# Kernel optimization log

Measured on AMD Instinct MI355X. Metric: run time of the kernel, lower is better.

Reference implementation:

```python
import jax, jax.numpy as jnp
import numpy as np
from jax import lax

EPS = 1e-6
D_MODEL = 2048
N_HEADS = 32
D_STATE = 64
HEADDIM = D_MODEL // N_HEADS  # 64, d_inner = expand*d_model = 2048
D_CONV = 4
INTER = 5504


def rmsnorm(x, w, eps=EPS):
    v = jnp.mean(jnp.square(x.astype(jnp.float32)), axis=-1, keepdims=True)
    return (x.astype(jnp.float32) * lax.rsqrt(v + eps)).astype(x.dtype) * w


def ssm_scan(x, dt, Bm, Cm):
    # x: (b,l,h,p) unscaled; dt: (b,l,h); Bm,Cm: (b,l,h,n)
    # DiscreteMamba2: h_t = exp(-dt_t) h_{t-1} + x_t (x) B_t ; y_t = h_t . C_t
    # (mamba_chunk_scan is called with x/dt and A=-1, so dt*(x/dt)=x)
    a = jnp.exp(-dt)  # (b,l,h)
    b, l, h, p = x.shape
    n = Bm.shape[-1]

    def step(hst, inp):
        a_t, x_t, B_t, C_t = inp
        hst = a_t[..., None, None] * hst + jnp.einsum('bhp,bhn->bhpn', x_t, B_t)
        y = jnp.einsum('bhpn,bhn->bhp', hst, C_t)
        return hst, y

    h0 = jnp.zeros((b, h, p, n), dtype=x.dtype)
    xs = (jnp.moveaxis(a, 1, 0), jnp.moveaxis(x, 1, 0),
          jnp.moveaxis(Bm, 1, 0), jnp.moveaxis(Cm, 1, 0))
    _, ys = lax.scan(step, h0, xs)
    return jnp.moveaxis(ys, 0, 1)  # (b,l,h,p)


def setup_inputs() -> dict:
    key = jax.random.key(0)
    ks = jax.random.split(key, 8)
    s = 0.02
    d_inner = D_MODEL
    conv_dim = d_inner + 2 * N_HEADS * D_STATE  # 6144
    d_in_proj = 2 * d_inner + 2 * N_HEADS * D_STATE + N_HEADS  # 8224
    return {
        'hidden_states': jax.random.normal(ks[0], (2, 2048, D_MODEL), jnp.float32),
        'attention_mask': jnp.ones((2, 2048), jnp.float32),
        'in_proj_w': jax.random.normal(ks[1], (d_in_proj, D_MODEL), jnp.float32) * s,
        'conv_w': jax.random.normal(ks[2], (conv_dim, 1, D_CONV), jnp.float32) * s,
        'conv_b': jnp.zeros((conv_dim,), jnp.float32),
        'z_bias': jnp.zeros((d_inner,), jnp.float32),
        'D': jnp.ones((N_HEADS,), jnp.float32),
        'out_proj_w': jax.random.normal(ks[3], (D_MODEL, d_inner), jnp.float32) * s,
        'ln1_w': jnp.ones((D_MODEL,), jnp.float32),
        'ln2_w': jnp.ones((D_MODEL,), jnp.float32),
        'gate_w': jax.random.normal(ks[4], (INTER, D_MODEL), jnp.float32) * s,
        'up_w': jax.random.normal(ks[5], (INTER, D_MODEL), jnp.float32) * s,
        'down_w': jax.random.normal(ks[6], (D_MODEL, INTER), jnp.float32) * s,
    }


def reference(hidden_states, attention_mask, in_proj_w, conv_w, conv_b, z_bias,
              D, out_proj_w, ln1_w, ln2_w, gate_w, up_w, down_w):
    b, l, d_model = hidden_states.shape
    d_inner = z_bias.shape[0]
    h_heads = D.shape[0]
    conv_dim = conv_w.shape[0]
    d_state = (conv_dim - d_inner) // (2 * h_heads)
    headdim = d_inner // h_heads

    residual = hidden_states
    h = rmsnorm(hidden_states, ln1_w)
    h = h * attention_mask[..., None]

    # --- DiscreteMamba2 mixer ---
    zxbcdt = jnp.einsum('bld,ed->ble', h, in_proj_w)
    z = zxbcdt[..., :d_inner]
    xBC = zxbcdt[..., d_inner:d_inner + conv_dim]
    A_log = zxbcdt[..., d_inner + conv_dim:]  # (b,l,h)

    # causal depthwise conv (activation = identity)
    xc = jnp.pad(jnp.swapaxes(xBC, 1, 2), ((0, 0), (0, 0), (conv_w.shape[-1] - 1, 0)))
    xBC = lax.conv_general_dilated(xc, conv_w, (1,), 'VALID',
                                   dimension_numbers=('NCH', 'OIH', 'NCH'),
                                   feature_group_count=conv_dim)
    xBC = jnp.swapaxes(xBC + conv_b[None, :, None], 1, 2)  # (b,l,conv_dim)

    x = xBC[..., :d_inner].reshape(b, l, h_heads, headdim)
    Bm = xBC[..., d_inner:d_inner + h_heads * d_state].reshape(b, l, h_heads, d_state)
    Cm = xBC[..., d_inner + h_heads * d_state:].reshape(b, l, h_heads, d_state)

    dt = jax.nn.softplus(A_log)  # (b,l,h)
    y = ssm_scan(x, dt, Bm, Cm)
    y = y + D[None, None, :, None] * x  # D skip uses unscaled x
    y = y.reshape(b, l, d_inner)

    gated = y * jax.nn.silu(z + z_bias)
    mixer_out = jnp.einsum('bld,ed->ble', gated, out_proj_w)

    h = mixer_out + residual
    residual2 = h
    h = rmsnorm(h, ln2_w)
    mlp = jnp.einsum('bli,di->bld',
                     jax.nn.silu(jnp.einsum('bld,id->bli', h, gate_w)) *
                     jnp.einsum('bld,id->bli', h, up_w),
                     down_w)
    return residual2 + mlp
```

## Files before the change

### kernel.cpp

```cpp
#include <hip/hip_runtime.h>
#include <math.h>

typedef __bf16 bf16_t;
typedef __attribute__((ext_vector_type(8))) __bf16 bf16x8;
typedef __attribute__((ext_vector_type(4))) float f32x4;

#define D_MODEL   2048
#define L_SEQ     2048
#define BATCH     2
#define NTOK      4096
#define N_HEADS   32
#define D_STATE   64
#define HEADDIM   64
#define D_INNER   2048
#define CONV_DIM  6144
#define D_IN_PROJ 8224
#define INTER     5504
#define QCHUNK    128
#define KCHUNKS   16

__device__ __forceinline__ void gld_lds16(const void* g, void* l) {
    __builtin_amdgcn_global_load_lds(
        (const __attribute__((address_space(1))) unsigned int*)g,
        (__attribute__((address_space(3))) unsigned int*)l, 16, 0, 0);
}

__global__ __launch_bounds__(256) void cvt_kernel(
    const float* __restrict__ s, bf16_t* __restrict__ d, int n8)
{
    int i = blockIdx.x * 256 + threadIdx.x;
    if (i >= n8) return;
    const float4* s4 = (const float4*)s;
    float4 a = s4[2 * i], b = s4[2 * i + 1];
    bf16x8 r;
    r[0] = (bf16_t)a.x; r[1] = (bf16_t)a.y; r[2] = (bf16_t)a.z; r[3] = (bf16_t)a.w;
    r[4] = (bf16_t)b.x; r[5] = (bf16_t)b.y; r[6] = (bf16_t)b.z; r[7] = (bf16_t)b.w;
    ((bf16x8*)d)[i] = r;
}

__global__ __launch_bounds__(256) void rmsnorm_kernel(
    const float* __restrict__ x, const float* __restrict__ w,
    const float* __restrict__ mask, bf16_t* __restrict__ out)
{
    __shared__ float red[4];
    __shared__ float sinv;
    int row = blockIdx.x;
    const float* xr = x + (size_t)row * D_MODEL;
    float xv[8];
    float ss = 0.f;
#pragma unroll
    for (int i = 0; i < 8; ++i) {
        float v = xr[threadIdx.x + 256 * i];
        xv[i] = v;
        ss += v * v;
    }
    for (int off = 32; off >= 1; off >>= 1) ss += __shfl_down(ss, off, 64);
    int lane = threadIdx.x & 63, wv = threadIdx.x >> 6;
    if (lane == 0) red[wv] = ss;
    __syncthreads();
    if (threadIdx.x == 0) {
        float t = red[0] + red[1] + red[2] + red[3];
        sinv = rsqrtf(t / (float)D_MODEL + 1e-6f);
    }
    __syncthreads();
    float s = sinv;
    float m = mask ? mask[row] : 1.f;
    bf16_t* orow = out + (size_t)row * D_MODEL;
#pragma unroll
    for (int i = 0; i < 8; ++i) {
        int c = threadIdx.x + 256 * i;
        orow[c] = (bf16_t)(xv[i] * s * w[c] * m);
    }
}

template <bool RES, typename OT>
__global__ __launch_bounds__(256) void gemm_bt(
    const bf16_t* __restrict__ X, const bf16_t* __restrict__ W,
    const float* __restrict__ R, OT* __restrict__ O,
    int N, int K)
{
    __shared__ __attribute__((aligned(16))) bf16_t As[128 * 32];
    __shared__ __attribute__((aligned(16))) bf16_t Bs[128 * 32];

    int tid = threadIdx.x;
    int m0 = blockIdx.y * 128;
    int n0 = blockIdx.x * 128;

    f32x4 acc[4][4] = {};

    int lane = tid & 63;
    int wv = tid >> 6;
    int wm = (wv >> 1) * 64, wn = (wv & 1) * 64;
    int lm = lane & 15, lq = lane >> 4;

    int srow = tid >> 2;
    int scol = (tid & 3) * 8;
    const bf16_t* Xp0 = X + (size_t)(m0 + srow) * K + scol;
    const bf16_t* Xp1 = X + (size_t)(m0 + 64 + srow) * K + scol;
    int wr0 = n0 + srow;      if (wr0 > N - 1) wr0 = N - 1;
    int wr1 = n0 + 64 + srow; if (wr1 > N - 1) wr1 = N - 1;
    const bf16_t* Wp0 = W + (size_t)wr0 * K + scol;
    const bf16_t* Wp1 = W + (size_t)wr1 * K + scol;
    bf16_t* lA0 = &As[tid * 8];
    bf16_t* lA1 = &As[2048 + tid * 8];
    bf16_t* lB0 = &Bs[tid * 8];
    bf16_t* lB1 = &Bs[2048 + tid * 8];

    for (int k0 = 0; k0 < K; k0 += 32) {
        __syncthreads();
        gld_lds16(Xp0 + k0, lA0);
        gld_lds16(Xp1 + k0, lA1);
        gld_lds16(Wp0 + k0, lB0);
        gld_lds16(Wp1 + k0, lB1);
        __syncthreads();

        bf16x8 a[4], b[4];
#pragma unroll
        for (int i = 0; i < 4; ++i)
            a[i] = *(const bf16x8*)&As[(wm + i * 16 + lm) * 32 + lq * 8];
#pragma unroll
        for (int i = 0; i < 4; ++i)
            b[i] = *(const bf16x8*)&Bs[(wn + i * 16 + lm) * 32 + lq * 8];
#pragma unroll
        for (int mi = 0; mi < 4; ++mi)
#pragma unroll
            for (int ni = 0; ni < 4; ++ni)
                acc[mi][ni] = __builtin_amdgcn_mfma_f32_16x16x32_bf16(
                    a[mi], b[ni], acc[mi][ni], 0, 0, 0);
    }

#pragma unroll
    for (int mi = 0; mi < 4; ++mi)
#pragma unroll
        for (int ni = 0; ni < 4; ++ni) {
            int n = n0 + wn + ni * 16 + lm;
            if (n >= N) continue;
            int mbase = m0 + wm + mi * 16 + lq * 4;
#pragma unroll
            for (int r = 0; r < 4; ++r) {
                size_t off = (size_t)(mbase + r) * N + n;
                float v = acc[mi][ni][r];
                if (RES) v += R[off];
                O[off] = (OT)v;
            }
        }
}

__global__ __launch_bounds__(256) void conv_kernel(
    const bf16_t* __restrict__ zx, const float* __restrict__ cw,
    const float* __restrict__ cb, bf16_t* __restrict__ out)
{
    int c = blockIdx.x * 256 + threadIdx.x;
    int l0 = blockIdx.y * 128;
    int b = blockIdx.z;
    float w0 = cw[c * 4 + 0], w1 = cw[c * 4 + 1];
    float w2 = cw[c * 4 + 2], w3 = cw[c * 4 + 3];
    float bias = cb[c];
    const bf16_t* src = zx + (size_t)b * L_SEQ * D_IN_PROJ + 2048 + c;
    bf16_t* dst = out + (size_t)b * L_SEQ * CONV_DIM + c;
    float xm3 = (l0 >= 3) ? (float)src[(size_t)(l0 - 3) * D_IN_PROJ] : 0.f;
    float xm2 = (l0 >= 2) ? (float)src[(size_t)(l0 - 2) * D_IN_PROJ] : 0.f;
    float xm1 = (l0 >= 1) ? (float)src[(size_t)(l0 - 1) * D_IN_PROJ] : 0.f;
    for (int l = l0; l < l0 + 128; ++l) {
        float xc = (float)src[(size_t)l * D_IN_PROJ];
        float r = bias + xm3 * w0 + xm2 * w1 + xm1 * w2 + xc * w3;
        dst[(size_t)l * CONV_DIM] = (bf16_t)r;
        xm3 = xm2; xm2 = xm1; xm1 = xc;
    }
}

__global__ __launch_bounds__(256) void scan_state_kernel(
    const bf16_t* __restrict__ conv, const bf16_t* __restrict__ zx,
    float* __restrict__ Schunk, float* __restrict__ Aprod)
{
    const int SS = 32;
    __shared__ __attribute__((aligned(16))) float xs[SS][64];
    __shared__ __attribute__((aligned(16))) float bs[SS][64];
    __shared__ float as_[SS];

    int k = blockIdx.x, h = blockIdx.y, b = blockIdx.z;
    int tid = threadIdx.x, lane = tid & 63, wv = tid >> 6;
    int pt = tid >> 3, nt = tid & 7;
    int p0 = pt * 2, n0 = nt * 8;

    float st0[8] = {0, 0, 0, 0, 0, 0, 0, 0};
    float st1[8] = {0, 0, 0, 0, 0, 0, 0, 0};
    float aprod = 1.f;

    const bf16_t* cbase = conv + (size_t)b * L_SEQ * CONV_DIM + h * 64;
    const bf16_t* abase = zx + (size_t)b * L_SEQ * D_IN_PROJ + 8192 + h;

    int tstart = k * QCHUNK;
    for (int t0 = tstart; t0 < tstart + QCHUNK; t0 += SS) {
        int soff = (wv >> 1) * 16;
        for (int s = 0; s < 16; ++s) {
            size_t row = (size_t)(t0 + soff + s);
            if ((wv & 1) == 0) xs[soff + s][lane] = (float)cbase[row * CONV_DIM + lane];
            else               bs[soff + s][lane] = (float)cbase[row * CONV_DIM + 2048 + lane];
        }
        if (tid < SS) {
            float v = (float)abase[(size_t)(t0 + tid) * D_IN_PROJ];
            as_[tid] = 1.f / (1.f + __expf(v));
        }
        __syncthreads();
        for (int s = 0; s < SS; ++s) {
            float a = as_[s];
            float x0 = xs[s][p0], x1 = xs[s][p0 + 1];
            aprod *= a;
#pragma unroll
            for (int j = 0; j < 8; ++j) {
                float Bv = bs[s][n0 + j];
                st0[j] = a * st0[j] + x0 * Bv;
                st1[j] = a * st1[j] + x1 * Bv;
            }
        }
        __syncthreads();
    }
    size_t base = (((size_t)(b * N_HEADS + h)) * KCHUNKS + k) * 4096;
    float4* d0 = (float4*)&Schunk[base + p0 * 64 + n0];
    d0[0] = make_float4(st0[0], st0[1], st0[2], st0[3]);
    d0[1] = make_float4(st0[4], st0[5], st0[6], st0[7]);
    float4* d1 = (float4*)&Schunk[base + (p0 + 1) * 64 + n0];
    d1[0] = make_float4(st1[0], st1[1], st1[2], st1[3]);
    d1[1] = make_float4(st1[4], st1[5], st1[6], st1[7]);
    if (tid == 0) Aprod[(b * N_HEADS + h) * KCHUNKS + k] = aprod;
}

__global__ __launch_bounds__(256) void scan_combine_kernel(
    const float* __restrict__ Schunk, const float* __restrict__ Aprod,
    float* __restrict__ Sinit)
{
    int bh = blockIdx.x >> 4;
    int e = (blockIdx.x & 15) * 256 + threadIdx.x;
    size_t base = (size_t)bh * KCHUNKS * 4096 + e;
    float S = 0.f;
    for (int k = 0; k < KCHUNKS; ++k) {
        Sinit[base + (size_t)k * 4096] = S;
        float ap = Aprod[bh * KCHUNKS + k];
        S = ap * S + Schunk[base + (size_t)k * 4096];
    }
}

__global__ __launch_bounds__(256) void scan_out_kernel(
    const bf16_t* __restrict__ conv, const bf16_t* __restrict__ zx,
    const float* __restrict__ Sinit, const float* __restrict__ Dp,
    const float* __restrict__ zb, bf16_t* __restrict__ gated)
{
    const int S = 16;
    __shared__ __attribute__((aligned(16))) float xs[S][64];
    __shared__ __attribute__((aligned(16))) float bs[S][64];
    __shared__ __attribute__((aligned(16))) float cs[S][64];
    __shared__ __attribute__((aligned(16))) float zs[S][64];
    __shared__ float as_[S];

    int k = blockIdx.x, h = blockIdx.y, b = blockIdx.z;
    int tid = threadIdx.x;
    int lane = tid & 63, wv = tid >> 6;
    int pt = tid >> 3, nt = tid & 7;
    int p0 = pt * 2, n0 = nt * 8;

    size_t sbase = (((size_t)(b * N_HEADS + h)) * KCHUNKS + k) * 4096;
    float4 v00 = *(const float4*)&Sinit[sbase + p0 * 64 + n0];
    float4 v01 = *(const float4*)&Sinit[sbase + p0 * 64 + n0 + 4];
    float4 v10 = *(const float4*)&Sinit[sbase + (p0 + 1) * 64 + n0];
    float4 v11 = *(const float4*)&Sinit[sbase + (p0 + 1) * 64 + n0 + 4];
    float st0[8] = {v00.x, v00.y, v00.z, v00.w, v01.x, v01.y, v01.z, v01.w};
    float st1[8] = {v10.x, v10.y, v10.z, v10.w, v11.x, v11.y, v11.z, v11.w};

    float Dh  = Dp[h];
    float zb0 = zb[h * 64 + p0];
    float zb1 = zb[h * 64 + p0 + 1];

    const bf16_t* cbase = conv + (size_t)b * L_SEQ * CONV_DIM + h * 64;
    const bf16_t* zbase = zx + (size_t)b * L_SEQ * D_IN_PROJ + h * 64;
    const bf16_t* abase = zx + (size_t)b * L_SEQ * D_IN_PROJ + 8192 + h;
    bf16_t* obase = gated + (size_t)b * L_SEQ * D_INNER + h * 64;

    int tstart = k * QCHUNK;
    for (int t0 = tstart; t0 < tstart + QCHUNK; t0 += S) {
        for (int s = 0; s < S; ++s) {
            size_t row = (size_t)(t0 + s);
            if (wv == 0)      xs[s][lane] = (float)cbase[row * CONV_DIM + lane];
            else if (wv == 1) bs[s][lane] = (float)cbase[row * CONV_DIM + 2048 + lane];
            else if (wv == 2) cs[s][lane] = (float)cbase[row * CONV_DIM + 4096 + lane];
            else              zs[s][lane] = (float)zbase[row * D_IN_PROJ + lane];
        }
        if (tid < S) {
            float v = (float)abase[(size_t)(t0 + tid) * D_IN_PROJ];
            as_[tid] = 1.f / (1.f + __expf(v));
        }
        __syncthreads();

        for (int s = 0; s < S; ++s) {
            float a = as_[s];
            float x0 = xs[s][p0], x1 = xs[s][p0 + 1];
            float part0 = 0.f, part1 = 0.f;
#pragma unroll
            for (int j = 0; j < 8; ++j) {
                float Bv = bs[s][n0 + j];
                float Cv = cs[s][n0 + j];
                st0[j] = a * st0[j] + x0 * Bv;
                st1[j] = a * st1[j] + x1 * Bv;
                part0 += st0[j] * Cv;
                part1 += st1[j] * Cv;
            }
            for (int o = 1; o < 8; o <<= 1) {
                part0 += __shfl_xor(part0, o, 64);
                part1 += __shfl_xor(part1, o, 64);
            }
            if (nt == 0) {
                float y0 = part0 + Dh * x0;
                float y1 = part1 + Dh * x1;
                float z0 = zs[s][p0] + zb0;
                float z1 = zs[s][p0 + 1] + zb1;
                y0 *= z0 / (1.f + __expf(-z0));
                y1 *= z1 / (1.f + __expf(-z1));
                bf16_t* o2 = obase + (size_t)(t0 + s) * D_INNER + p0;
                o2[0] = (bf16_t)y0;
                o2[1] = (bf16_t)y1;
            }
        }
        __syncthreads();
    }
}

__global__ __launch_bounds__(256) void act_kernel(
    const bf16x8* __restrict__ g, const bf16x8* __restrict__ u,
    bf16x8* __restrict__ act, int n8)
{
    int i = blockIdx.x * 256 + threadIdx.x;
    if (i >= n8) return;
    bf16x8 gv = g[i], uv = u[i], r;
#pragma unroll
    for (int j = 0; j < 8; ++j) {
        float x = (float)gv[j];
        r[j] = (bf16_t)((x / (1.f + __expf(-x))) * (float)uv[j]);
    }
    act[i] = r;
}

extern "C" void kernel_launch(void* const* d_in, const int* in_sizes, int n_in,
                              void* d_out, int out_size, void* d_ws, size_t ws_size,
                              hipStream_t stream) {
    const float* hidden     = (const float*)d_in[0];
    const float* mask       = (const float*)d_in[1];
    const float* in_proj_w  = (const float*)d_in[2];
    const float* conv_w     = (const float*)d_in[3];
    const float* conv_b     = (const float*)d_in[4];
    const float* z_bias     = (const float*)d_in[5];
    const float* Dvec       = (const float*)d_in[6];
    const float* out_proj_w = (const float*)d_in[7];
    const float* ln1_w      = (const float*)d_in[8];
    const float* ln2_w      = (const float*)d_in[9];
    const float* gate_w     = (const float*)d_in[10];
    const float* up_w       = (const float*)d_in[11];
    const float* down_w     = (const float*)d_in[12];
    float* out = (float*)d_out;

    char* ws = (char*)d_ws;
    bf16_t* zxb    = (bf16_t*)(ws + 0);
    bf16_t* convo  = (bf16_t*)(ws + 67371008);
    bf16_t* hn     = (bf16_t*)(ws + 117702656);
    bf16_t* gated  = (bf16_t*)(ws + 117702656);
    bf16_t* h2n    = (bf16_t*)(ws + 134479872);
    float*  Schunk = (float*) (ws + 134479872);
    bf16_t* wbuf   = (bf16_t*)(ws + 151257088);
    float*  Sinit  = (float*) (ws + 151257088);
    float*  Aprod  = (float*) (ws + 168034304);
    bf16_t* gbuf   = (bf16_t*)(ws + 0);
    bf16_t* ubuf   = (bf16_t*)(ws + 45088768);

    rmsnorm_kernel<<<NTOK, 256, 0, stream>>>(hidden, ln1_w, mask, hn);
    cvt_kernel<<<8224, 256, 0, stream>>>(in_proj_w, wbuf, D_IN_PROJ * D_MODEL / 8);
    gemm_bt<false, bf16_t><<<dim3(65, 32), 256, 0, stream>>>(hn, wbuf, nullptr, zxb, D_IN_PROJ, D_MODEL);
    conv_kernel<<<dim3(24, 16, 2), 256, 0, stream>>>(zxb, conv_w, conv_b, convo);
    scan_state_kernel<<<dim3(KCHUNKS, N_HEADS, BATCH), 256, 0, stream>>>(convo, zxb, Schunk, Aprod);
    scan_combine_kernel<<<1024, 256, 0, stream>>>(Schunk, Aprod, Sinit);
    scan_out_kernel<<<dim3(KCHUNKS, N_HEADS, BATCH), 256, 0, stream>>>(convo, zxb, Sinit, Dvec, z_bias, gated);
    cvt_kernel<<<2048, 256, 0, stream>>>(out_proj_w, wbuf, D_MODEL * D_INNER / 8);
    gemm_bt<true, float><<<dim3(16, 32), 256, 0, stream>>>(gated, wbuf, hidden, out, D_MODEL, D_INNER);
    rmsnorm_kernel<<<NTOK, 256, 0, stream>>>(out, ln2_w, nullptr, h2n);
    cvt_kernel<<<5504, 256, 0, stream>>>(gate_w, wbuf, INTER * D_MODEL / 8);
    gemm_bt<false, bf16_t><<<dim3(43, 32), 256, 0, stream>>>(h2n, wbuf, nullptr, gbuf, INTER, D_MODEL);
    cvt_kernel<<<5504, 256, 0, stream>>>(up_w, wbuf, INTER * D_MODEL / 8);
    gemm_bt<false, bf16_t><<<dim3(43, 32), 256, 0, stream>>>(h2n, wbuf, nullptr, ubuf, INTER, D_MODEL);
    act_kernel<<<11008, 256, 0, stream>>>(
        (const bf16x8*)gbuf, (const bf16x8*)ubuf, (bf16x8*)gbuf, NTOK * INTER / 8);
    cvt_kernel<<<5504, 256, 0, stream>>>(down_w, wbuf, D_MODEL * INTER / 8);
    gemm_bt<true, float><<<dim3(16, 32), 256, 0, stream>>>(gbuf, wbuf, out, out, D_MODEL, INTER);
}
```

Baseline: 1.170 ms.

## Add 256x256 pipelined GEMM kernel and fuse gate/up projections into one GEMM

Adds a new 512-thread GEMM with 256x256 tiles. It uses direct global-to-LDS loads, a multi-stage software pipeline with explicit waitcnt and barriers, XCD-aware block remapping and MFMA priority hints. The new kernel handles most of in_proj and a single fused gate+up GEMM over concatenated weights, and the small in_proj tail still goes through the old kernel. The fused GEMM cuts one pass over the activations and one launch, at the cost of a strided act kernel and a more fragile hand-scheduled pipeline with large register use.

```diff
diff --git a/kernel.cpp b/kernel.cpp
--- a/kernel.cpp
+++ b/kernel.cpp
@@ -77,7 +77,7 @@
 __global__ __launch_bounds__(256) void gemm_bt(
     const bf16_t* __restrict__ X, const bf16_t* __restrict__ W,
     const float* __restrict__ R, OT* __restrict__ O,
-    int N, int K)
+    int N, int K, int ldo)
 {
     __shared__ __attribute__((aligned(16))) bf16_t As[128 * 32];
     __shared__ __attribute__((aligned(16))) bf16_t Bs[128 * 32];
@@ -138,7 +138,175 @@
             int mbase = m0 + wm + mi * 16 + lq * 4;
 #pragma unroll
             for (int r = 0; r < 4; ++r) {
-                size_t off = (size_t)(mbase + r) * N + n;
+                size_t off = (size_t)(mbase + r) * ldo + n;
+                float v = acc[mi][ni][r];
+                if (RES) v += R[off];
+                O[off] = (OT)v;
+            }
+        }
+}
+
+
+#define G8_BARRIER() do { asm volatile("" ::: "memory"); \
+    __builtin_amdgcn_s_barrier(); \
+    asm volatile("" ::: "memory"); } while (0)
+#define G8_LGKM0() do { asm volatile("s_waitcnt lgkmcnt(0)" ::: "memory"); \
+    __builtin_amdgcn_sched_barrier(0); } while (0)
+#define G8_VMCNT(n) asm volatile("s_waitcnt vmcnt(" #n ")" ::: "memory")
+
+template <int C>
+__device__ __forceinline__ void g8_stage(
+    int t, int nt4, const bf16_t* pA, size_t hK64,
+    const bf16_t* pB0, const bf16_t* pB1, const bf16_t* pB2, const bf16_t* pB3,
+    unsigned dbase, bf16_t* lds)
+{
+    constexpr int w = C & 3;
+    constexpr unsigned so = (((C >> 2) & 1) ? 65536u : 0u) + (unsigned)w * 16384u;
+    int j = 8 * t + C;
+    if (j >= nt4) return;
+    size_t goff = (size_t)(j >> 2) * 64;
+    const bf16_t *g0, *g1;
+    if constexpr (w == 0)      { g0 = pA;              g1 = pA + hK64; }
+    else if constexpr (w == 1) { g0 = pA + 2 * hK64;   g1 = pA + 3 * hK64; }
+    else if constexpr (w == 2) { g0 = pB0;             g1 = pB1; }
+    else                       { g0 = pB2;             g1 = pB3; }
+    gld_lds16(g0 + goff, (char*)lds + (so + dbase));
+    gld_lds16(g1 + goff, (char*)lds + (so + 8192u + dbase));
+}
+
+template <bool RES, typename OT>
+__global__ __launch_bounds__(512, 2) void gemm8p(
+    const bf16_t* __restrict__ X, const bf16_t* __restrict__ W,
+    const float* __restrict__ R, OT* __restrict__ O,
+    int N, int K, int ldo)
+{
+    __shared__ __attribute__((aligned(1024))) bf16_t lds[65536];
+
+    const int tid  = threadIdx.x;
+    const int lane = tid & 63;
+    const int wid  = tid >> 6;
+    const int wr   = wid >> 2;
+    const int wc   = wid & 3;
+
+    int nx   = gridDim.x;
+    int nwg  = nx * gridDim.y;
+    int orig = blockIdx.x + nx * blockIdx.y;
+    int qx = nwg >> 3, rx = nwg & 7;
+    int xcd = orig & 7, l8 = orig >> 3;
+    int wg = (xcd < rx ? xcd * (qx + 1) : rx * (qx + 1) + (xcd - rx) * qx) + l8;
+    int m0 = (wg / nx) * 256;
+    int n0 = (wg % nx) * 256;
+
+    const int NT    = K >> 6;
+    const int nt4   = NT << 2;
+    const int niter = NT >> 1;
+
+    int lrow = ((tid >> 7) << 4) + ((tid >> 2) & 15);
+    int cb   = (tid & 3) * 16;
+    int cblg = cb ^ (((tid >> 2) & 8) ? 32 : 0);
+    int lcol = (((tid >> 6) & 1) << 5) + (cblg >> 1);
+    const size_t hK64 = (size_t)K << 6;
+    const bf16_t* pA = X + (size_t)(m0 + lrow) * K + lcol;
+    const bf16_t* pB[4];
+#pragma unroll
+    for (int hi = 0; hi < 4; ++hi) {
+        int rw = n0 + (hi >> 1) * 128 + (hi & 1) * 64 + lrow;
+        if (rw > N - 1) rw = N - 1;
+        pB[hi] = W + (size_t)rw * K + lcol;
+    }
+    const unsigned dbase = (unsigned)tid * 16u;
+
+    unsigned c2s = ((unsigned)(lane >> 4) << 4) ^ ((lane & 8) ? 32u : 0u);
+    unsigned rdA = (unsigned)(wr * 16384 + (lane & 15) * 64) + c2s;
+    unsigned rdB = 32768u + (unsigned)((wc >> 1) * 16384 + (wc & 1) * 8192
+                                       + (lane & 15) * 64) + c2s;
+
+    f32x4 acc[8][4] = {};
+    bf16x8 a[8][2], b[4][2];
+
+#define G8_STG(C) g8_stage<C>(t, nt4, pA, hK64, pB[0], pB[1], pB[2], pB[3], dbase, lds)
+#define G8_LDFRAGS(SO) do { \
+    const char* pa_ = (const char*)lds + (SO) + rdA; \
+    const char* pb_ = (const char*)lds + (SO) + rdB; \
+    _Pragma("unroll") for (int mi = 0; mi < 8; ++mi) { \
+        a[mi][0] = *(const bf16x8*)(pa_ + mi * 2048); \
+        a[mi][1] = *(const bf16x8*)(pa_ + mi * 2048 + 1024); } \
+    _Pragma("unroll") for (int ni = 0; ni < 4; ++ni) { \
+        b[ni][0] = *(const bf16x8*)(pb_ + ni * 2048); \
+        b[ni][1] = *(const bf16x8*)(pb_ + ni * 2048 + 1024); } \
+} while (0)
+#define G8_MFMAQ(MI0, NI0) do { \
+    __builtin_amdgcn_s_setprio(1); \
+    _Pragma("unroll") for (int mi = 0; mi < 4; ++mi) \
+    _Pragma("unroll") for (int ni = 0; ni < 2; ++ni) \
+    _Pragma("unroll") for (int ks = 0; ks < 2; ++ks) \
+        acc[(MI0) + mi][(NI0) + ni] = __builtin_amdgcn_mfma_f32_16x16x32_bf16( \
+            a[(MI0) + mi][ks], b[(NI0) + ni][ks], acc[(MI0) + mi][(NI0) + ni], 0, 0, 0); \
+    __builtin_amdgcn_s_setprio(0); \
+} while (0)
+
+    {
+        int t = 0;
+        G8_STG(0); G8_STG(1); G8_STG(2); G8_STG(3);
+        G8_STG(4); G8_STG(5); G8_STG(6);
+    }
+    G8_VMCNT(6);
+    G8_BARRIER();
+
+#pragma unroll 1
+    for (int t = 0; t < niter; ++t) {
+        G8_STG(7);
+        G8_LDFRAGS(0u);
+        G8_BARRIER(); G8_LGKM0();
+        G8_MFMAQ(0, 0);
+        G8_BARRIER();
+        G8_STG(8);
+        G8_BARRIER();
+        G8_MFMAQ(0, 2);
+        G8_BARRIER();
+        G8_STG(9);
+        G8_BARRIER();
+        G8_MFMAQ(4, 0);
+        G8_BARRIER();
+        G8_STG(10);
+        if (t == niter - 1) { G8_VMCNT(0); } else { G8_VMCNT(6); }
+        G8_BARRIER();
+        G8_MFMAQ(4, 2);
+        G8_BARRIER();
+        G8_STG(11);
+        G8_LDFRAGS(65536u);
+        G8_BARRIER(); G8_LGKM0();
+        G8_MFMAQ(0, 0);
+        G8_BARRIER();
+        G8_STG(12);
+        G8_BARRIER();
+        G8_MFMAQ(0, 2);
+        G8_BARRIER();
+        G8_STG(13);
+        G8_BARRIER();
+        G8_MFMAQ(4, 0);
+        G8_BARRIER();
+        G8_STG(14);
+        G8_VMCNT(6);
+        G8_BARRIER();
+        G8_MFMAQ(4, 2);
+        G8_BARRIER();
+    }
+
+#undef G8_STG
+#undef G8_LDFRAGS
+#undef G8_MFMAQ
+
+#pragma unroll
+    for (int mi = 0; mi < 8; ++mi)
+#pragma unroll
+        for (int ni = 0; ni < 4; ++ni) {
+            int n = n0 + wc * 64 + ni * 16 + (lane & 15);
+            if (n >= N) continue;
+            int mbase = m0 + wr * 128 + mi * 16 + (lane >> 4) * 4;
+#pragma unroll
+            for (int r = 0; r < 4; ++r) {
+                size_t off = (size_t)(mbase + r) * ldo + n;
                 float v = acc[mi][ni][r];
                 if (RES) v += R[off];
                 O[off] = (OT)v;
@@ -325,18 +493,21 @@
 }
 
 __global__ __launch_bounds__(256) void act_kernel(
-    const bf16x8* __restrict__ g, const bf16x8* __restrict__ u,
-    bf16x8* __restrict__ act, int n8)
+    const bf16_t* __restrict__ gu, bf16_t* __restrict__ act, int n8)
 {
     int i = blockIdx.x * 256 + threadIdx.x;
     if (i >= n8) return;
-    bf16x8 gv = g[i], uv = u[i], r;
+    int row = i / (INTER / 8);
+    int c8  = i % (INTER / 8);
+    const bf16x8* g = (const bf16x8*)(gu + (size_t)row * (2 * INTER)) + c8;
+    const bf16x8* u = (const bf16x8*)(gu + (size_t)row * (2 * INTER) + INTER) + c8;
+    bf16x8 gv = *g, uv = *u, r;
 #pragma unroll
     for (int j = 0; j < 8; ++j) {
         float x = (float)gv[j];
         r[j] = (bf16_t)((x / (1.f + __expf(-x))) * (float)uv[j]);
     }
-    act[i] = r;
+    ((bf16x8*)act)[i] = r;
 }
 
 extern "C" void kernel_launch(void* const* d_in, const int* in_sizes, int n_in,
@@ -362,30 +533,36 @@
     bf16_t* convo  = (bf16_t*)(ws + 67371008);
     bf16_t* hn     = (bf16_t*)(ws + 117702656);
     bf16_t* gated  = (bf16_t*)(ws + 117702656);
-    bf16_t* h2n    = (bf16_t*)(ws + 134479872);
     float*  Schunk = (float*) (ws + 134479872);
     bf16_t* wbuf   = (bf16_t*)(ws + 151257088);
     float*  Sinit  = (float*) (ws + 151257088);
     float*  Aprod  = (float*) (ws + 168034304);
-    bf16_t* gbuf   = (bf16_t*)(ws + 0);
-    bf16_t* ubuf   = (bf16_t*)(ws + 45088768);
+    bf16_t* guO    = (bf16_t*)(ws + 0);
+    bf16_t* guW    = (bf16_t*)(ws + 90177536);
+    bf16_t* actO   = (bf16_t*)(ws + 90177536);
+    bf16_t* h2n    = (bf16_t*)(ws + 135266304);
+    bf16_t* dwW    = (bf16_t*)(ws + 135266304);
 
     rmsnorm_kernel<<<NTOK, 256, 0, stream>>>(hidden, ln1_w, mask, hn);
     cvt_kernel<<<8224, 256, 0, stream>>>(in_proj_w, wbuf, D_IN_PROJ * D_MODEL / 8);
-    gemm_bt<false, bf16_t><<<dim3(65, 32), 256, 0, stream>>>(hn, wbuf, nullptr, zxb, D_IN_PROJ, D_MODEL);
+    gemm8p<false, bf16_t><<<dim3(32, 16), 512, 0, stream>>>(
+        hn, wbuf, nullptr, zxb, 8192, D_MODEL, D_IN_PROJ);
+    gemm_bt<false, bf16_t><<<dim3(1, 32), 256, 0, stream>>>(
+        hn, wbuf + (size_t)8192 * D_MODEL, nullptr, zxb + 8192, 32, D_MODEL, D_IN_PROJ);
     conv_kernel<<<dim3(24, 16, 2), 256, 0, stream>>>(zxb, conv_w, conv_b, convo);
     scan_state_kernel<<<dim3(KCHUNKS, N_HEADS, BATCH), 256, 0, stream>>>(convo, zxb, Schunk, Aprod);
     scan_combine_kernel<<<1024, 256, 0, stream>>>(Schunk, Aprod, Sinit);
     scan_out_kernel<<<dim3(KCHUNKS, N_HEADS, BATCH), 256, 0, stream>>>(convo, zxb, Sinit, Dvec, z_bias, gated);
     cvt_kernel<<<2048, 256, 0, stream>>>(out_proj_w, wbuf, D_MODEL * D_INNER / 8);
-    gemm_bt<true, float><<<dim3(16, 32), 256, 0, stream>>>(gated, wbuf, hidden, out, D_MODEL, D_INNER);
+    gemm_bt<true, float><<<dim3(16, 32), 256, 0, stream>>>(
+        gated, wbuf, hidden, out, D_MODEL, D_INNER, D_MODEL);
     rmsnorm_kernel<<<NTOK, 256, 0, stream>>>(out, ln2_w, nullptr, h2n);
-    cvt_kernel<<<5504, 256, 0, stream>>>(gate_w, wbuf, INTER * D_MODEL / 8);
-    gemm_bt<false, bf16_t><<<dim3(43, 32), 256, 0, stream>>>(h2n, wbuf, nullptr, gbuf, INTER, D_MODEL);
-    cvt_kernel<<<5504, 256, 0, stream>>>(up_w, wbuf, INTER * D_MODEL / 8);
-    gemm_bt<false, bf16_t><<<dim3(43, 32), 256, 0, stream>>>(h2n, wbuf, nullptr, ubuf, INTER, D_MODEL);
-    act_kernel<<<11008, 256, 0, stream>>>(
-        (const bf16x8*)gbuf, (const bf16x8*)ubuf, (bf16x8*)gbuf, NTOK * INTER / 8);
-    cvt_kernel<<<5504, 256, 0, stream>>>(down_w, wbuf, D_MODEL * INTER / 8);
-    gemm_bt<true, float><<<dim3(16, 32), 256, 0, stream>>>(gbuf, wbuf, out, out, D_MODEL, INTER);
-}
+    cvt_kernel<<<5504, 256, 0, stream>>>(gate_w, guW, INTER * D_MODEL / 8);
+    cvt_kernel<<<5504, 256, 0, stream>>>(up_w, guW + (size_t)INTER * D_MODEL, INTER * D_MODEL / 8);
+    gemm8p<false, bf16_t><<<dim3(43, 16), 512, 0, stream>>>(
+        h2n, guW, nullptr, guO, 2 * INTER, D_MODEL, 2 * INTER);
+    act_kernel<<<11008, 256, 0, stream>>>(guO, actO, NTOK * INTER / 8);
+    cvt_kernel<<<5504, 256, 0, stream>>>(down_w, dwW, D_MODEL * INTER / 8);
+    gemm_bt<true, float><<<dim3(16, 32), 256, 0, stream>>>(
+        actO, dwW, out, out, D_MODEL, INTER, D_MODEL);
+}
```

Measured after the change: 1.176 ms. About the same (+0.5%).
